# Performance work log

Measured on AMD Instinct MI355X. Metric: run time of the kernel, lower is better.

The kernel has to match this reference:

```python
import jax, jax.numpy as jnp
import numpy as np

NUM_HEADS = 12
HEAD_DIM = 64
DIM = 768


def _rot_interleaved(t):
    # rot(x): pairs (x0,x1) -> (-x1, x0), interleaved layout
    x1 = t[..., ::2]
    x2 = t[..., 1::2]
    return jnp.stack([-x2, x1], axis=-1).reshape(t.shape)


def _apply_rope_cat(t, emb):
    # emb: [N, 2*head_dim] = concat(sin, cos); t: [B, H, N, head_dim]
    sin_e, cos_e = jnp.split(emb, 2, axis=-1)  # each [N, head_dim]
    return t * cos_e + _rot_interleaved(t) * sin_e


def setup_inputs() -> dict:
    key = jax.random.key(0)
    ks = jax.random.split(key, 8)
    B, Nq, Nkv = 16, 256, 4096
    s = 1.0 / np.sqrt(DIM)
    return {
        "x": jax.random.normal(ks[0], (B, Nq, DIM), dtype=jnp.float32),
        "context": jax.random.normal(ks[1], (B, Nkv, DIM), dtype=jnp.float32),
        "rope_q": jax.random.normal(ks[2], (Nq, 2 * HEAD_DIM), dtype=jnp.float32),
        "rope_k": jax.random.normal(ks[3], (Nkv, 2 * HEAD_DIM), dtype=jnp.float32),
        "Wq": jax.random.normal(ks[4], (DIM, DIM), dtype=jnp.float32) * s,
        "Wk": jax.random.normal(ks[5], (DIM, DIM), dtype=jnp.float32) * s,
        "Wv": jax.random.normal(ks[6], (DIM, DIM), dtype=jnp.float32) * s,
        "Wo": jax.random.normal(ks[7], (DIM, DIM), dtype=jnp.float32) * s,
    }


def reference(x, context, rope_q, rope_k, Wq, Wk, Wv, Wo):
    B, Nq, _ = x.shape
    Nkv = context.shape[1]
    H, hd = NUM_HEADS, HEAD_DIM
    scale = hd ** -0.5

    # projections -> [B, H, N, hd]
    q = jnp.einsum('bnd,df->bnf', x, Wq).reshape(B, Nq, H, hd).transpose(0, 2, 1, 3)
    k = jnp.einsum('bnd,df->bnf', context, Wk).reshape(B, Nkv, H, hd).transpose(0, 2, 1, 3)
    v = jnp.einsum('bnd,df->bnf', context, Wv).reshape(B, Nkv, H, hd).transpose(0, 2, 1, 3)

    q = _apply_rope_cat(q, rope_q)
    k = _apply_rope_cat(k, rope_k)

    attn = jnp.einsum('bhqd,bhkd->bhqk', q * scale, k)
    attn = jax.nn.softmax(attn, axis=-1)
    o = jnp.einsum('bhqk,bhkd->bhqd', attn, v)  # [B, H, Nq, hd]
    o = o.transpose(0, 2, 1, 3).reshape(B, Nq, H * hd)
    return jnp.einsum('bnf,fo->bno', o, Wo)
```

## Files before the change

kernel.cpp:

```cpp
#include <hip/hip_runtime.h>
#include <stdint.h>


typedef __bf16 bf16x8 __attribute__((ext_vector_type(8)));
typedef unsigned short u16x8 __attribute__((ext_vector_type(8)));
typedef unsigned short u16x4 __attribute__((ext_vector_type(4)));
typedef uint32_t u32x4 __attribute__((ext_vector_type(4)));
typedef float f32x4 __attribute__((ext_vector_type(4)));

#define DIMF 768
#define NHEAD 12
#define NKV 4096
#define NQ 256
#define NB 16

struct alignas(8) us4 { unsigned short x, y, z, w; };

__device__ __forceinline__ unsigned short f2bf(float x) {
  uint32_t u = __float_as_uint(x);
  u += 0x7fffu + ((u >> 16) & 1u);
  return (unsigned short)(u >> 16);
}

__device__ __forceinline__ uint32_t cvtpk(float a, float b) {
  uint32_t r;
  asm("v_cvt_pk_bf16_f32 %0, %1, %2" : "=v"(r) : "v"(a), "v"(b));
  return r;
}

__device__ __forceinline__ void gld_lds16(const unsigned short* g, unsigned short* l) {
  __builtin_amdgcn_global_load_lds(
      (const __attribute__((address_space(1))) uint32_t*)(uintptr_t)g,
      (__attribute__((address_space(3))) uint32_t*)(uintptr_t)l, 16, 0, 0);
}

__global__ void cvt_kernel(const float* __restrict__ in, unsigned short* __restrict__ out, int n) {
  int stride = gridDim.x * blockDim.x * 4;
  for (int i = (blockIdx.x * blockDim.x + threadIdx.x) * 4; i < n; i += stride) {
    float4 v = *(const float4*)(in + i);
    us4 o{f2bf(v.x), f2bf(v.y), f2bf(v.z), f2bf(v.w)};
    *(us4*)(out + i) = o;
  }
}

__global__ void twt_kernel(const float* __restrict__ W0, const float* __restrict__ W1,
                           const float* __restrict__ W2, const float* __restrict__ W3,
                           unsigned short* __restrict__ O0, unsigned short* __restrict__ O1,
                           unsigned short* __restrict__ O2, unsigned short* __restrict__ O3) {
  const float* W; unsigned short* O;
  switch (blockIdx.z) {
    case 0: W = W0; O = O0; break;
    case 1: W = W1; O = O1; break;
    case 2: W = W2; O = O2; break;
    default: W = W3; O = O3; break;
  }
  __shared__ float t[32][33];
  int x0 = blockIdx.x * 32, y0 = blockIdx.y * 32;
  int tx = threadIdx.x, ty = threadIdx.y;
#pragma unroll
  for (int j = 0; j < 4; ++j)
    t[ty + 8 * j][tx] = W[(size_t)(y0 + ty + 8 * j) * DIMF + x0 + tx];
  __syncthreads();
#pragma unroll
  for (int j = 0; j < 4; ++j)
    O[(size_t)(x0 + ty + 8 * j) * DIMF + y0 + tx] = f2bf(t[tx][ty + 8 * j]);
}

template <int MODE>
__launch_bounds__(256, 2)
__global__ void kvgemm_kernel(const unsigned short* __restrict__ A,
                              const unsigned short* __restrict__ Bt,
                              void* __restrict__ outp,
                              const float* __restrict__ rope) {
  __shared__ unsigned short As[256 * 64];
  __shared__ unsigned short Bs[128 * 64];
  const int t = threadIdx.x;
  const int lane = t & 63, wid = t >> 6;
  const int g = lane >> 4, lc = lane & 15;
  const int wr = wid >> 1, wc = wid & 1;

  const int swz = (blockIdx.x & 7) * 192 + (blockIdx.x >> 3);
  const int rowBase = (swz / 6) * 256;
  const int colBase = (swz % 6) * 128;

  const f32x4 z4 = {0.f, 0.f, 0.f, 0.f};
  f32x4 acc[8][4];
#pragma unroll
  for (int m = 0; m < 8; ++m)
#pragma unroll
    for (int n = 0; n < 4; ++n) acc[m][n] = z4;

  const int sr = lane >> 3;
  const int sc = (lane & 7) ^ sr;
  const unsigned short* Abase = A + (size_t)(rowBase + wid * 8 + sr) * DIMF + sc * 8;
  const unsigned short* Bbase = Bt + (size_t)(colBase + wid * 8 + sr) * DIMF + sc * 8;

  for (int kb = 0; kb < 12; ++kb) {
    __syncthreads();
#pragma unroll
    for (int i = 0; i < 8; ++i)
      gld_lds16(Abase + (size_t)i * 32 * DIMF + kb * 64, &As[(i * 32 + wid * 8) * 64]);
#pragma unroll
    for (int i = 0; i < 4; ++i)
      gld_lds16(Bbase + (size_t)i * 32 * DIMF + kb * 64, &Bs[(i * 32 + wid * 8) * 64]);
    __syncthreads();
#pragma unroll
    for (int kk = 0; kk < 2; ++kk) {
      bf16x8 af[8], bfr[4];
#pragma unroll
      for (int m = 0; m < 8; ++m) {
        int row = wr * 128 + m * 16 + lc;
        af[m] = *(const bf16x8*)&As[row * 64 + (((kk * 4 + g) ^ (row & 7)) << 3)];
      }
#pragma unroll
      for (int n = 0; n < 4; ++n) {
        int row = wc * 64 + n * 16 + lc;
        bfr[n] = *(const bf16x8*)&Bs[row * 64 + (((kk * 4 + g) ^ (row & 7)) << 3)];
      }
#pragma unroll
      for (int m = 0; m < 8; ++m)
#pragma unroll
        for (int n = 0; n < 4; ++n)
          acc[m][n] = __builtin_amdgcn_mfma_f32_16x16x32_bf16(af[m], bfr[n], acc[m][n], 0, 0, 0);
    }
  }

  if (MODE == 0) {
    unsigned short* Ko = (unsigned short*)outp;
#pragma unroll
    for (int m = 0; m < 8; ++m)
#pragma unroll
      for (int n = 0; n < 4; ++n)
#pragma unroll
        for (int r = 0; r < 4; ++r) {
          int p = rowBase + wr * 128 + m * 16 + g * 4 + r;
          int f = colBase + wc * 64 + n * 16 + lc;
          int d = f & 63, h = f >> 6;
          float v = acc[m][n][r];
          float vo = __shfl_xor(v, 1);
          int b = p >> 12, nkv = p & 4095;
          float sn = rope[nkv * 128 + d], cs = rope[nkv * 128 + 64 + d];
          float o = (d & 1) ? fmaf(vo, sn, v * cs) : fmaf(-vo, sn, v * cs);
          Ko[((size_t)(b * NHEAD + h) * NKV + nkv) * 64 + d] = f2bf(o);
        }
  } else {
    unsigned short* Vt = (unsigned short*)outp;
#pragma unroll
    for (int m = 0; m < 8; ++m)
#pragma unroll
      for (int n = 0; n < 4; ++n) {
        int p0 = rowBase + wr * 128 + m * 16 + g * 4;
        int b = p0 >> 12, nkv0 = p0 & 4095;
        int f = colBase + wc * 64 + n * 16 + lc;
        int d = f & 63, h = f >> 6;
        us4 wv{f2bf(acc[m][n][0]), f2bf(acc[m][n][1]), f2bf(acc[m][n][2]), f2bf(acc[m][n][3])};
        *(us4*)&Vt[((size_t)(b * NHEAD + h) * 64 + d) * NKV + nkv0] = wv;
      }
  }
}

template <int MODE>
__launch_bounds__(256, 2)
__global__ void gemm_kernel(const unsigned short* __restrict__ A,
                            const unsigned short* __restrict__ Bt,
                            void* __restrict__ outp,
                            const float* __restrict__ rope) {
  __shared__ unsigned short As[128 * 64];
  __shared__ unsigned short Bs[128 * 64];
  const int t = threadIdx.x;
  const int lane = t & 63, wid = t >> 6;
  const int g = lane >> 4, lc = lane & 15;
  const int wr = wid >> 1, wc = wid & 1;
  const int rowBase = blockIdx.x * 128, colBase = blockIdx.y * 128;

  const f32x4 z4 = {0.f, 0.f, 0.f, 0.f};
  f32x4 acc[4][4];
#pragma unroll
  for (int m = 0; m < 4; ++m)
#pragma unroll
    for (int n = 0; n < 4; ++n) acc[m][n] = z4;

  const int r0 = t >> 3;
  const int c0 = t & 7;

  bf16x8 ra[4], rbx[4];
#pragma unroll
  for (int pp = 0; pp < 4; ++pp) {
    int row = pp * 32 + r0;
    ra[pp] = *(const bf16x8*)(A + (size_t)(rowBase + row) * DIMF + c0 * 8);
    rbx[pp] = *(const bf16x8*)(Bt + (size_t)(colBase + row) * DIMF + c0 * 8);
  }

  for (int kb = 0; kb < 12; ++kb) {
    __syncthreads();
#pragma unroll
    for (int pp = 0; pp < 4; ++pp) {
      int row = pp * 32 + r0;
      int ph = ((c0 ^ (row & 7)) << 3);
      *(bf16x8*)&As[row * 64 + ph] = ra[pp];
      *(bf16x8*)&Bs[row * 64 + ph] = rbx[pp];
    }
    __syncthreads();
    if (kb + 1 < 12) {
      int kn = (kb + 1) * 64;
#pragma unroll
      for (int pp = 0; pp < 4; ++pp) {
        int row = pp * 32 + r0;
        ra[pp] = *(const bf16x8*)(A + (size_t)(rowBase + row) * DIMF + kn + c0 * 8);
        rbx[pp] = *(const bf16x8*)(Bt + (size_t)(colBase + row) * DIMF + kn + c0 * 8);
      }
    }
#pragma unroll
    for (int kk = 0; kk < 2; ++kk) {
      bf16x8 af[4], bfr[4];
#pragma unroll
      for (int m = 0; m < 4; ++m) {
        int row = wr * 64 + m * 16 + lc;
        int ch = kk * 4 + g;
        af[m] = *(const bf16x8*)&As[row * 64 + (((ch ^ (row & 7))) << 3)];
      }
#pragma unroll
      for (int n = 0; n < 4; ++n) {
        int row = wc * 64 + n * 16 + lc;
        int ch = kk * 4 + g;
        bfr[n] = *(const bf16x8*)&Bs[row * 64 + (((ch ^ (row & 7))) << 3)];
      }
#pragma unroll
      for (int m = 0; m < 4; ++m)
#pragma unroll
        for (int n = 0; n < 4; ++n)
          acc[m][n] = __builtin_amdgcn_mfma_f32_16x16x32_bf16(af[m], bfr[n], acc[m][n], 0, 0, 0);
    }
  }

  if (MODE == 2) {
    unsigned short* Ko = (unsigned short*)outp;
#pragma unroll
    for (int m = 0; m < 4; ++m)
#pragma unroll
      for (int n = 0; n < 4; ++n)
#pragma unroll
        for (int r = 0; r < 4; ++r) {
          int p = rowBase + wr * 64 + m * 16 + g * 4 + r;
          int f = colBase + wc * 64 + n * 16 + lc;
          int d = f & 63, h = f >> 6;
          float v = acc[m][n][r];
          float vo = __shfl_xor(v, 1);
          int b = p >> 8, nq = p & 255;
          float sn = rope[nq * 128 + d], cs = rope[nq * 128 + 64 + d];
          float o = (d & 1) ? fmaf(vo, sn, v * cs) : fmaf(-vo, sn, v * cs);
          Ko[((size_t)(b * NHEAD + h) * NQ + nq) * 64 + d] = f2bf(o * 0.125f);
        }
  } else {
    float* Co = (float*)outp;
#pragma unroll
    for (int m = 0; m < 4; ++m)
#pragma unroll
      for (int n = 0; n < 4; ++n)
#pragma unroll
        for (int r = 0; r < 4; ++r) {
          int p = rowBase + wr * 64 + m * 16 + g * 4 + r;
          int f = colBase + wc * 64 + n * 16 + lc;
          Co[(size_t)p * DIMF + f] = acc[m][n][r];
        }
  }
}

__launch_bounds__(256, 2)
__global__ void attn_kernel(const unsigned short* __restrict__ Qb,
                            const unsigned short* __restrict__ Kb,
                            const unsigned short* __restrict__ Vtb,
                            unsigned short* __restrict__ Ob) {
  __shared__ unsigned short Ks[128 * 64];
  __shared__ unsigned short Vts[64 * 128];
  const int logical = (blockIdx.x & 7) * 96 + (blockIdx.x >> 3);
  const int qt = logical & 3, bh = logical >> 2;
  const int b = bh / NHEAD, h = bh % NHEAD;
  const int t = threadIdx.x;
  const int lane = t & 63, w = t >> 6;
  const int g = lane >> 4, lc = lane & 15;
  const int qrow = qt * 64 + w * 16 + lc;

  bf16x8 qf[2];
#pragma unroll
  for (int kk = 0; kk < 2; ++kk)
    qf[kk] = *(const bf16x8*)(Qb + ((size_t)bh * NQ + qrow) * 64 + kk * 32 + g * 8);

  const f32x4 z4 = {0.f, 0.f, 0.f, 0.f};
  f32x4 oacc[4];
#pragma unroll
  for (int df = 0; df < 4; ++df) oacc[df] = z4;
  float mrun = -1e30f, lrun = 0.f;

  const int r0 = t >> 3, c0 = t & 7;
  const int d0 = t >> 4, cv = t & 15;
  const int pbase = 32 * (cv >> 2) + 16 * (cv & 1) + 4 * ((cv >> 1) & 1);
  const int ch0 = pbase >> 3, of0 = pbase & 7;
  const int ch1 = (pbase + 8) >> 3;

  u16x8 rk[4], rv[4];
#define LOAD_TILE(KT)                                                                        \
  do {                                                                                       \
    const int kvb = (KT) * 128;                                                              \
    _Pragma("unroll")                                                                        \
    for (int pp = 0; pp < 4; ++pp)                                                           \
      rk[pp] = *(const u16x8*)(Kb + ((size_t)bh * NKV + kvb + pp * 32 + r0) * 64 + c0 * 8);  \
    _Pragma("unroll")                                                                        \
    for (int pp = 0; pp < 4; ++pp)                                                           \
      rv[pp] = *(const u16x8*)(Vtb + ((size_t)bh * 64 + pp * 16 + d0) * NKV + kvb + cv * 8); \
  } while (0)

  LOAD_TILE(0);

  for (int kt = 0; kt < 32; ++kt) {
    __syncthreads();
#pragma unroll
    for (int pp = 0; pp < 4; ++pp) {
      int row = pp * 32 + r0;
      *(u16x8*)&Ks[row * 64 + ((c0 ^ (row & 7)) << 3)] = rk[pp];
    }
#pragma unroll
    for (int pp = 0; pp < 4; ++pp) {
      int d = pp * 16 + d0;
      u16x4 lo = __builtin_shufflevector(rv[pp], rv[pp], 0, 1, 2, 3);
      u16x4 hi = __builtin_shufflevector(rv[pp], rv[pp], 4, 5, 6, 7);
      *(u16x4*)&Vts[d * 128 + ((ch0 ^ (d & 15)) << 3) + of0] = lo;
      *(u16x4*)&Vts[d * 128 + ((ch1 ^ (d & 15)) << 3) + of0] = hi;
    }
    if (kt + 1 < 32) LOAD_TILE(kt + 1);
    __syncthreads();

    f32x4 s[8];
#pragma unroll
    for (int c = 0; c < 8; ++c) s[c] = z4;
#pragma unroll
    for (int kk = 0; kk < 2; ++kk)
#pragma unroll
      for (int c = 0; c < 8; ++c) {
        int row = c * 16 + lc;
        bf16x8 kf = *(const bf16x8*)&Ks[row * 64 + (((kk * 4 + g) ^ (row & 7)) << 3)];
        s[c] = __builtin_amdgcn_mfma_f32_16x16x32_bf16(kf, qf[kk], s[c], 0, 0, 0);
      }

    float mx = s[0][0];
#pragma unroll
    for (int c = 0; c < 8; ++c)
#pragma unroll
      for (int r = 0; r < 4; ++r) mx = fmaxf(mx, s[c][r]);
    mx = fmaxf(mx, __shfl_xor(mx, 16));
    mx = fmaxf(mx, __shfl_xor(mx, 32));
    float nm = fmaxf(mrun, mx);
    float al = __expf(mrun - nm);
    mrun = nm;
    float ls = 0.f;
#pragma unroll
    for (int c = 0; c < 8; ++c)
#pragma unroll
      for (int r = 0; r < 4; ++r) {
        float p = __expf(s[c][r] - nm);
        s[c][r] = p;
        ls += p;
      }
    ls += __shfl_xor(ls, 16);
    ls += __shfl_xor(ls, 32);
    lrun = lrun * al + ls;
#pragma unroll
    for (int df = 0; df < 4; ++df)
#pragma unroll
      for (int r = 0; r < 4; ++r) oacc[df][r] *= al;

    uint32_t pk[8][2];
#pragma unroll
    for (int c = 0; c < 8; ++c)
#pragma unroll
      for (int w2 = 0; w2 < 2; ++w2)
        pk[c][w2] = cvtpk(s[c][2 * w2], s[c][2 * w2 + 1]);

#pragma unroll
    for (int kb = 0; kb < 4; ++kb) {
      u32x4 pw = {pk[2 * kb][0], pk[2 * kb][1], pk[2 * kb + 1][0], pk[2 * kb + 1][1]};
      bf16x8 pa = __builtin_bit_cast(bf16x8, pw);
#pragma unroll
      for (int df = 0; df < 4; ++df) {
        int row = df * 16 + lc;
        bf16x8 vf = *(const bf16x8*)&Vts[row * 128 + (((kb * 4 + g) ^ (row & 15)) << 3)];
        oacc[df] = __builtin_amdgcn_mfma_f32_16x16x32_bf16(vf, pa, oacc[df], 0, 0, 0);
      }
    }
  }
#undef LOAD_TILE

  float inv = 1.0f / lrun;
#pragma unroll
  for (int df = 0; df < 4; ++df) {
    us4 wv{f2bf(oacc[df][0] * inv), f2bf(oacc[df][1] * inv),
           f2bf(oacc[df][2] * inv), f2bf(oacc[df][3] * inv)};
    *(us4*)&Ob[((size_t)b * NQ + qrow) * DIMF + h * 64 + df * 16 + g * 4] = wv;
  }
}

extern "C" void kernel_launch(void* const* d_in, const int* in_sizes, int n_in,
                              void* d_out, int out_size, void* d_ws, size_t ws_size,
                              hipStream_t stream) {
  const float* x      = (const float*)d_in[0];
  const float* ctx    = (const float*)d_in[1];
  const float* rope_q = (const float*)d_in[2];
  const float* rope_k = (const float*)d_in[3];
  const float* Wq     = (const float*)d_in[4];
  const float* Wk     = (const float*)d_in[5];
  const float* Wv     = (const float*)d_in[6];
  const float* Wo     = (const float*)d_in[7];

  char* ws = (char*)d_ws;
  const size_t SZ_CTXB = (size_t)NB * NKV * DIMF * 2;
  const size_t SZ_XB   = (size_t)NB * NQ * DIMF * 2;
  const size_t SZ_WT   = (size_t)DIMF * DIMF * 2;
  unsigned short* ctxb = (unsigned short*)(ws);
  unsigned short* ob   = (unsigned short*)(ws);
  unsigned short* xb   = (unsigned short*)(ws + SZ_CTXB);
  unsigned short* wkt  = (unsigned short*)(ws + SZ_CTXB + SZ_XB);
  unsigned short* wvt  = (unsigned short*)(ws + SZ_CTXB + SZ_XB + SZ_WT);
  unsigned short* wqt  = (unsigned short*)(ws + SZ_CTXB + SZ_XB + 2 * SZ_WT);
  unsigned short* wot  = (unsigned short*)(ws + SZ_CTXB + SZ_XB + 3 * SZ_WT);
  unsigned short* kb   = (unsigned short*)(ws + SZ_CTXB + SZ_XB + 4 * SZ_WT);
  unsigned short* vtb  = (unsigned short*)(ws + SZ_CTXB + SZ_XB + 4 * SZ_WT + SZ_CTXB);
  unsigned short* qb   = (unsigned short*)(ws + SZ_CTXB + SZ_XB + 4 * SZ_WT + 2 * SZ_CTXB);

  cvt_kernel<<<dim3(2048), dim3(256), 0, stream>>>(ctx, ctxb, NB * NKV * DIMF);
  cvt_kernel<<<dim3(1024), dim3(256), 0, stream>>>(x, xb, NB * NQ * DIMF);
  twt_kernel<<<dim3(24, 24, 4), dim3(32, 8), 0, stream>>>(Wk, Wv, Wq, Wo, wkt, wvt, wqt, wot);

  kvgemm_kernel<0><<<dim3(1536), dim3(256), 0, stream>>>(ctxb, wkt, kb, rope_k);
  kvgemm_kernel<1><<<dim3(1536), dim3(256), 0, stream>>>(ctxb, wvt, vtb, nullptr);
  gemm_kernel<2><<<dim3(32, 6), dim3(256), 0, stream>>>(xb, wqt, qb, rope_q);

  attn_kernel<<<dim3(768), dim3(256), 0, stream>>>(qb, kb, vtb, ob);

  gemm_kernel<3><<<dim3(32, 6), dim3(256), 0, stream>>>(ob, wot, d_out, nullptr);
}
```

Measured before the change: 407.4 us.

## Double-buffer K/V projection GEMM with async LDS prefetch and smaller tiles

Rewrites the K/V projection GEMM to use a two-stage LDS double buffer. The global-to-LDS loads for k-block kb+2 are issued while block kb is computed, and vmcnt waits replace full syncthreads. The tile shrinks from 256x128 to 128x128 so two buffers fit in LDS, and the grid doubles to 3072 blocks with an adjusted swizzle. The aim is to hide global load latency behind MFMA work, at the cost of less operand reuse per block and more total B-tile traffic.

```diff
diff --git a/kernel.cpp b/kernel.cpp
--- a/kernel.cpp
+++ b/kernel.cpp
@@ -68,72 +68,89 @@
 
 template <int MODE>
 __launch_bounds__(256, 2)
-__global__ void kvgemm_kernel(const unsigned short* __restrict__ A,
+__global__ void kvpipe_kernel(const unsigned short* __restrict__ A,
                               const unsigned short* __restrict__ Bt,
                               void* __restrict__ outp,
                               const float* __restrict__ rope) {
-  __shared__ unsigned short As[256 * 64];
-  __shared__ unsigned short Bs[128 * 64];
+  __shared__ unsigned short As[2][128 * 64];
+  __shared__ unsigned short Bs[2][128 * 64];
   const int t = threadIdx.x;
   const int lane = t & 63, wid = t >> 6;
   const int g = lane >> 4, lc = lane & 15;
   const int wr = wid >> 1, wc = wid & 1;
 
-  const int swz = (blockIdx.x & 7) * 192 + (blockIdx.x >> 3);
-  const int rowBase = (swz / 6) * 256;
+  const int swz = (blockIdx.x & 7) * 384 + (blockIdx.x >> 3);
+  const int rowBase = (swz / 6) * 128;
   const int colBase = (swz % 6) * 128;
 
   const f32x4 z4 = {0.f, 0.f, 0.f, 0.f};
-  f32x4 acc[8][4];
-#pragma unroll
-  for (int m = 0; m < 8; ++m)
+  f32x4 acc[4][4];
+#pragma unroll
+  for (int m = 0; m < 4; ++m)
 #pragma unroll
     for (int n = 0; n < 4; ++n) acc[m][n] = z4;
 
   const int sr = lane >> 3;
   const int sc = (lane & 7) ^ sr;
-  const unsigned short* Abase = A + (size_t)(rowBase + wid * 8 + sr) * DIMF + sc * 8;
-  const unsigned short* Bbase = Bt + (size_t)(colBase + wid * 8 + sr) * DIMF + sc * 8;
-
+  const unsigned short* Abase = A + (size_t)(rowBase + wid * 32 + sr) * DIMF + sc * 8;
+  const unsigned short* Bbase = Bt + (size_t)(colBase + wid * 32 + sr) * DIMF + sc * 8;
+
+#define STAGE(KB, BUF)                                                                     \
+  do {                                                                                     \
+    _Pragma("unroll")                                                                      \
+    for (int i = 0; i < 4; ++i) {                                                          \
+      gld_lds16(Abase + (size_t)(i * 8) * DIMF + (KB) * 64, &As[BUF][(wid * 32 + i * 8) * 64]); \
+      gld_lds16(Bbase + (size_t)(i * 8) * DIMF + (KB) * 64, &Bs[BUF][(wid * 32 + i * 8) * 64]); \
+    }                                                                                      \
+  } while (0)
+
+  STAGE(0, 0);
+  STAGE(1, 1);
+
+#pragma unroll
   for (int kb = 0; kb < 12; ++kb) {
-    __syncthreads();
-#pragma unroll
-    for (int i = 0; i < 8; ++i)
-      gld_lds16(Abase + (size_t)i * 32 * DIMF + kb * 64, &As[(i * 32 + wid * 8) * 64]);
-#pragma unroll
-    for (int i = 0; i < 4; ++i)
-      gld_lds16(Bbase + (size_t)i * 32 * DIMF + kb * 64, &Bs[(i * 32 + wid * 8) * 64]);
-    __syncthreads();
+    const int c = kb & 1;
+    if (kb < 11) {
+      asm volatile("s_waitcnt vmcnt(8)" ::: "memory");
+    } else {
+      asm volatile("s_waitcnt vmcnt(0)" ::: "memory");
+    }
+    __builtin_amdgcn_s_barrier();
+    asm volatile("" ::: "memory");
 #pragma unroll
     for (int kk = 0; kk < 2; ++kk) {
-      bf16x8 af[8], bfr[4];
-#pragma unroll
-      for (int m = 0; m < 8; ++m) {
-        int row = wr * 128 + m * 16 + lc;
-        af[m] = *(const bf16x8*)&As[row * 64 + (((kk * 4 + g) ^ (row & 7)) << 3)];
+      bf16x8 af[4], bfr[4];
+#pragma unroll
+      for (int m = 0; m < 4; ++m) {
+        int row = wr * 64 + m * 16 + lc;
+        af[m] = *(const bf16x8*)&As[c][row * 64 + (((kk * 4 + g) ^ (row & 7)) << 3)];
       }
 #pragma unroll
       for (int n = 0; n < 4; ++n) {
         int row = wc * 64 + n * 16 + lc;
-        bfr[n] = *(const bf16x8*)&Bs[row * 64 + (((kk * 4 + g) ^ (row & 7)) << 3)];
-      }
-#pragma unroll
-      for (int m = 0; m < 8; ++m)
+        bfr[n] = *(const bf16x8*)&Bs[c][row * 64 + (((kk * 4 + g) ^ (row & 7)) << 3)];
+      }
+#pragma unroll
+      for (int m = 0; m < 4; ++m)
 #pragma unroll
         for (int n = 0; n < 4; ++n)
           acc[m][n] = __builtin_amdgcn_mfma_f32_16x16x32_bf16(af[m], bfr[n], acc[m][n], 0, 0, 0);
     }
-  }
+    asm volatile("" ::: "memory");
+    __builtin_amdgcn_s_barrier();
+    if (kb + 2 < 12) STAGE(kb + 2, c);
+  }
+#undef STAGE
 
   if (MODE == 0) {
     unsigned short* Ko = (unsigned short*)outp;
 #pragma unroll
-    for (int m = 0; m < 8; ++m)
+    for (int m = 0; m < 4; ++m)
 #pragma unroll
       for (int n = 0; n < 4; ++n)
 #pragma unroll
         for (int r = 0; r < 4; ++r) {
-          int p = rowBase + wr * 128 + m * 16 + g * 4 + r;
+          int p = rowBase + wr * 64 + m * 16 + g * 4 + r;
           int f = colBase + wc * 64 + n * 16 + lc;
           int d = f & 63, h = f >> 6;
           float v = acc[m][n][r];
@@ -146,10 +163,10 @@
   } else {
     unsigned short* Vt = (unsigned short*)outp;
 #pragma unroll
-    for (int m = 0; m < 8; ++m)
+    for (int m = 0; m < 4; ++m)
 #pragma unroll
       for (int n = 0; n < 4; ++n) {
-        int p0 = rowBase + wr * 128 + m * 16 + g * 4;
+        int p0 = rowBase + wr * 64 + m * 16 + g * 4;
         int b = p0 >> 12, nkv0 = p0 & 4095;
         int f = colBase + wc * 64 + n * 16 + lc;
         int d = f & 63, h = f >> 6;
@@ -430,8 +447,8 @@
   cvt_kernel<<<dim3(1024), dim3(256), 0, stream>>>(x, xb, NB * NQ * DIMF);
   twt_kernel<<<dim3(24, 24, 4), dim3(32, 8), 0, stream>>>(Wk, Wv, Wq, Wo, wkt, wvt, wqt, wot);
 
-  kvgemm_kernel<0><<<dim3(1536), dim3(256), 0, stream>>>(ctxb, wkt, kb, rope_k);
-  kvgemm_kernel<1><<<dim3(1536), dim3(256), 0, stream>>>(ctxb, wvt, vtb, nullptr);
+  kvpipe_kernel<0><<<dim3(3072), dim3(256), 0, stream>>>(ctxb, wkt, kb, rope_k);
+  kvpipe_kernel<1><<<dim3(3072), dim3(256), 0, stream>>>(ctxb, wvt, vtb, nullptr);
   gemm_kernel<2><<<dim3(32, 6), dim3(256), 0, stream>>>(xb, wqt, qb, rope_q);
 
   attn_kernel<<<dim3(768), dim3(256), 0, stream>>>(qb, kb, vtb, ob);
```

Result: slower. 453.7 us (+11.4%).

## Fuse K and V projections into one double-buffered 256x256-tile GEMM kernel

Applied to the files above, without the earlier changes.

Replaces the two separate K and V projection launches with one kernel that treats the adjacent wkt/wvt buffers as a single 1536-column weight. It uses 256x256 tiles with 8 waves and 128KB of dynamic LDS, double-buffered across K steps. Global-to-LDS loads are issued in quarter-steps interleaved with MFMA work, using explicit vmcnt waits, barriers and setprio. The aim is to read the context tile once for both K and V and to hide load latency. The cost is heavy LDS use, which limits occupancy to one block per CU, and a reliance on wvt sitting immediately after wkt in the workspace.

```diff
diff --git a/kernel.cpp b/kernel.cpp
--- a/kernel.cpp
+++ b/kernel.cpp
@@ -66,75 +66,117 @@
     O[(size_t)(x0 + ty + 8 * j) * DIMF + y0 + tx] = f2bf(t[tx][ty + 8 * j]);
 }
 
-template <int MODE>
-__launch_bounds__(256, 2)
-__global__ void kvgemm_kernel(const unsigned short* __restrict__ A,
-                              const unsigned short* __restrict__ Bt,
-                              void* __restrict__ outp,
-                              const float* __restrict__ rope) {
-  __shared__ unsigned short As[256 * 64];
-  __shared__ unsigned short Bs[128 * 64];
+__launch_bounds__(512, 2)
+__global__ void kv8_kernel(const unsigned short* __restrict__ A,
+                           const unsigned short* __restrict__ Bkv,
+                           unsigned short* __restrict__ Ko,
+                           unsigned short* __restrict__ Vt,
+                           const float* __restrict__ rope) {
+  extern __shared__ unsigned short smem[];
   const int t = threadIdx.x;
   const int lane = t & 63, wid = t >> 6;
   const int g = lane >> 4, lc = lane & 15;
-  const int wr = wid >> 1, wc = wid & 1;
+  const int wr = wid >> 2, wc = wid & 3;
 
   const int swz = (blockIdx.x & 7) * 192 + (blockIdx.x >> 3);
   const int rowBase = (swz / 6) * 256;
-  const int colBase = (swz % 6) * 128;
-
-  const f32x4 z4 = {0.f, 0.f, 0.f, 0.f};
+  const int colBase = (swz % 6) * 256;
+
   f32x4 acc[8][4];
 #pragma unroll
   for (int m = 0; m < 8; ++m)
 #pragma unroll
-    for (int n = 0; n < 4; ++n) acc[m][n] = z4;
+    for (int n = 0; n < 4; ++n)
+#pragma unroll
+      for (int r = 0; r < 4; ++r) acc[m][n][r] = 0.f;
 
   const int sr = lane >> 3;
   const int sc = (lane & 7) ^ sr;
-  const unsigned short* Abase = A + (size_t)(rowBase + wid * 8 + sr) * DIMF + sc * 8;
-  const unsigned short* Bbase = Bt + (size_t)(colBase + wid * 8 + sr) * DIMF + sc * 8;
-
-  for (int kb = 0; kb < 12; ++kb) {
-    __syncthreads();
-#pragma unroll
-    for (int i = 0; i < 8; ++i)
-      gld_lds16(Abase + (size_t)i * 32 * DIMF + kb * 64, &As[(i * 32 + wid * 8) * 64]);
-#pragma unroll
-    for (int i = 0; i < 4; ++i)
-      gld_lds16(Bbase + (size_t)i * 32 * DIMF + kb * 64, &Bs[(i * 32 + wid * 8) * 64]);
-    __syncthreads();
-#pragma unroll
-    for (int kk = 0; kk < 2; ++kk) {
-      bf16x8 af[8], bfr[4];
-#pragma unroll
-      for (int m = 0; m < 8; ++m) {
-        int row = wr * 128 + m * 16 + lc;
-        af[m] = *(const bf16x8*)&As[row * 64 + (((kk * 4 + g) ^ (row & 7)) << 3)];
-      }
-#pragma unroll
-      for (int n = 0; n < 4; ++n) {
-        int row = wc * 64 + n * 16 + lc;
-        bfr[n] = *(const bf16x8*)&Bs[row * 64 + (((kk * 4 + g) ^ (row & 7)) << 3)];
-      }
-#pragma unroll
-      for (int m = 0; m < 8; ++m)
-#pragma unroll
-        for (int n = 0; n < 4; ++n)
-          acc[m][n] = __builtin_amdgcn_mfma_f32_16x16x32_bf16(af[m], bfr[n], acc[m][n], 0, 0, 0);
-    }
-  }
-
-  if (MODE == 0) {
-    unsigned short* Ko = (unsigned short*)outp;
+  const unsigned short* Abase0 = A + (size_t)(rowBase + wid * 16 + sr) * DIMF + sc * 8;
+  const unsigned short* Bbase0 = Bkv + (size_t)(colBase + wid * 16 + sr) * DIMF + sc * 8;
+
+#define STAGE_A(T, h)                                                              \
+  do {                                                                             \
+    unsigned short* _lb = smem + (((T) & 1) * 2 + (h)) * 8192;                     \
+    const unsigned short* _gb = Abase0 + (size_t)(h) * 128 * DIMF + (T) * 64;      \
+    gld_lds16(_gb, _lb + (wid * 16) * 64);                                         \
+    gld_lds16(_gb + (size_t)8 * DIMF, _lb + (wid * 16 + 8) * 64);                  \
+  } while (0)
+#define STAGE_B(T, h)                                                              \
+  do {                                                                             \
+    unsigned short* _lb = smem + 32768 + (((T) & 1) * 2 + (h)) * 8192;             \
+    const unsigned short* _gb = Bbase0 + (size_t)(h) * 128 * DIMF + (T) * 64;      \
+    gld_lds16(_gb, _lb + (wid * 16) * 64);                                         \
+    gld_lds16(_gb + (size_t)8 * DIMF, _lb + (wid * 16 + 8) * 64);                  \
+  } while (0)
+
+  STAGE_A(0, 0); STAGE_B(0, 0); STAGE_B(0, 1); STAGE_A(0, 1);
+  STAGE_A(1, 0); STAGE_B(1, 0);
+
+  bf16x8 af[4][2], bfr[2][2];
+
+  for (int T = 0; T < 12; ++T) {
+    const int dbuf = T & 1;
+    if (T == 11) asm volatile("s_waitcnt vmcnt(0)" ::: "memory");
+    else         asm volatile("s_waitcnt vmcnt(4)" ::: "memory");
+    asm volatile("" ::: "memory");
+    __builtin_amdgcn_s_barrier();
+    asm volatile("" ::: "memory");
+
+#pragma unroll
+    for (int q = 0; q < 4; ++q) {
+      const int ah = q >> 1, bh = q & 1;
+      const unsigned short* Ab = smem + (dbuf * 2 + ah) * 8192;
+      const unsigned short* Bb = smem + 32768 + (dbuf * 2 + bh) * 8192;
+      if ((q & 1) == 0) {
+#pragma unroll
+        for (int mp = 0; mp < 4; ++mp)
+#pragma unroll
+          for (int kk = 0; kk < 2; ++kk) {
+            int row = mp * 32 + wr * 16 + lc;
+            af[mp][kk] = *(const bf16x8*)&Ab[row * 64 + (((kk * 4 + g) ^ (row & 7)) << 3)];
+          }
+      }
+#pragma unroll
+      for (int np = 0; np < 2; ++np)
+#pragma unroll
+        for (int kk = 0; kk < 2; ++kk) {
+          int row = np * 64 + wc * 16 + lc;
+          bfr[np][kk] = *(const bf16x8*)&Bb[row * 64 + (((kk * 4 + g) ^ (row & 7)) << 3)];
+        }
+      if (q == 0)      { if (T + 1 < 12) STAGE_B(T + 1, 1); }
+      else if (q == 1) { if (T + 1 < 12) STAGE_A(T + 1, 1); }
+      else if (q == 2) { if (T + 2 < 12) STAGE_A(T + 2, 0); }
+      else             { if (T + 2 < 12) STAGE_B(T + 2, 0); }
+      asm volatile("" ::: "memory");
+      __builtin_amdgcn_s_barrier();
+      asm volatile("s_waitcnt lgkmcnt(0)" ::: "memory");
+      __builtin_amdgcn_s_setprio(1);
+#pragma unroll
+      for (int mp = 0; mp < 4; ++mp)
+#pragma unroll
+        for (int np = 0; np < 2; ++np)
+#pragma unroll
+          for (int kk = 0; kk < 2; ++kk)
+            acc[4 * ah + mp][2 * bh + np] = __builtin_amdgcn_mfma_f32_16x16x32_bf16(
+                af[mp][kk], bfr[np][kk], acc[4 * ah + mp][2 * bh + np], 0, 0, 0);
+      __builtin_amdgcn_s_setprio(0);
+      asm volatile("" ::: "memory");
+      __builtin_amdgcn_s_barrier();
+    }
+  }
+#undef STAGE_A
+#undef STAGE_B
+
+  if (colBase < 768) {
 #pragma unroll
     for (int m = 0; m < 8; ++m)
 #pragma unroll
       for (int n = 0; n < 4; ++n)
 #pragma unroll
         for (int r = 0; r < 4; ++r) {
-          int p = rowBase + wr * 128 + m * 16 + g * 4 + r;
-          int f = colBase + wc * 64 + n * 16 + lc;
+          int p = rowBase + m * 32 + wr * 16 + g * 4 + r;
+          int f = colBase + n * 64 + wc * 16 + lc;
           int d = f & 63, h = f >> 6;
           float v = acc[m][n][r];
           float vo = __shfl_xor(v, 1);
@@ -144,14 +186,13 @@
           Ko[((size_t)(b * NHEAD + h) * NKV + nkv) * 64 + d] = f2bf(o);
         }
   } else {
-    unsigned short* Vt = (unsigned short*)outp;
 #pragma unroll
     for (int m = 0; m < 8; ++m)
 #pragma unroll
       for (int n = 0; n < 4; ++n) {
-        int p0 = rowBase + wr * 128 + m * 16 + g * 4;
+        int p0 = rowBase + m * 32 + wr * 16 + g * 4;
         int b = p0 >> 12, nkv0 = p0 & 4095;
-        int f = colBase + wc * 64 + n * 16 + lc;
+        int f = (colBase - 768) + n * 64 + wc * 16 + lc;
         int d = f & 63, h = f >> 6;
         us4 wv{f2bf(acc[m][n][0]), f2bf(acc[m][n][1]), f2bf(acc[m][n][2]), f2bf(acc[m][n][3])};
         *(us4*)&Vt[((size_t)(b * NHEAD + h) * 64 + d) * NKV + nkv0] = wv;
@@ -430,8 +471,7 @@
   cvt_kernel<<<dim3(1024), dim3(256), 0, stream>>>(x, xb, NB * NQ * DIMF);
   twt_kernel<<<dim3(24, 24, 4), dim3(32, 8), 0, stream>>>(Wk, Wv, Wq, Wo, wkt, wvt, wqt, wot);
 
-  kvgemm_kernel<0><<<dim3(1536), dim3(256), 0, stream>>>(ctxb, wkt, kb, rope_k);
-  kvgemm_kernel<1><<<dim3(1536), dim3(256), 0, stream>>>(ctxb, wvt, vtb, nullptr);
+  kv8_kernel<<<dim3(1536), dim3(512), 131072, stream>>>(ctxb, wkt, kb, vtb, rope_k);
   gemm_kernel<2><<<dim3(32, 6), dim3(256), 0, stream>>>(xb, wqt, qb, rope_q);
 
   attn_kernel<<<dim3(768), dim3(256), 0, stream>>>(qb, kb, vtb, ob);
```

Result: faster. 390.6 us (-4.1%).
